# Optimization experiments

Hardware: AMD Instinct MI355X
Metric: run time of the kernel (lower is better)

## Reference

```python
import jax, jax.numpy as jnp
import numpy as np

C = 343.0                      # wave speed
OMEGA = 2.0 * np.pi * 1000.0   # angular frequency
K2 = (C / OMEGA) ** 2          # coefficient on u in the (as-written) residual

N_POINTS = 262144
HIDDEN = 256


def _mlp_point(p, W1, b1, W2, b2, W3, b3, W4, b4):
    # p: (3,) -> scalar u(x,y,z); tanh MLP stand-in for model_estimation
    h = jnp.tanh(p @ W1 + b1)
    h = jnp.tanh(h @ W2 + b2)
    h = jnp.tanh(h @ W3 + b3)
    return (h @ W4 + b4)[0]


def setup_inputs() -> dict:
    key = jax.random.key(0)
    ks = jax.random.split(key, 5)

    def init_w(k, fan_in, fan_out):
        return jax.random.normal(k, (fan_in, fan_out), dtype=jnp.float32) / np.sqrt(fan_in).astype(np.float32)

    inputs = jax.random.normal(ks[0], (N_POINTS, 3), dtype=jnp.float32)
    W1 = init_w(ks[1], 3, HIDDEN)
    W2 = init_w(ks[2], HIDDEN, HIDDEN)
    W3 = init_w(ks[3], HIDDEN, HIDDEN)
    W4 = init_w(ks[4], HIDDEN, 1)
    z = lambda n: jnp.zeros((n,), dtype=jnp.float32)
    return {
        "inputs": inputs,
        "W1": W1, "b1": z(HIDDEN),
        "W2": W2, "b2": z(HIDDEN),
        "W3": W3, "b3": z(HIDDEN),
        "W4": W4, "b4": z(1),
    }


def reference(inputs, W1, b1, W2, b2, W3, b3, W4, b4):
    # Per-point scalar field u(p); Laplacian = trace of the 3x3 Hessian.
    def u_point(p):
        return _mlp_point(p, W1, b1, W2, b2, W3, b3, W4, b4)

    u = jax.vmap(u_point)(inputs)                       # [N]
    hess = jax.vmap(jax.hessian(u_point))(inputs)       # [N, 3, 3]
    laplace_u = hess[:, 0, 0] + hess[:, 1, 1] + hess[:, 2, 2]  # [N]

    pde_residual = laplace_u + K2 * u
    return jnp.mean(jnp.abs(pde_residual) ** 2)
```

## Files before the change

kernel.cpp:

```cpp
#include <hip/hip_runtime.h>
#include <math.h>

#define HID 256
#define PTS 16
#define NSTR 5
#define ROWS (NSTR*PTS)
#define PITCH 272

typedef _Float16 half4v __attribute__((ext_vector_type(4)));
typedef _Float16 half8  __attribute__((ext_vector_type(8)));
typedef float   floatx4 __attribute__((ext_vector_type(4)));

constexpr double PI_D = 3.14159265358979323846;
constexpr float K2F = (float)((343.0/(2.0*PI_D*1000.0))*(343.0/(2.0*PI_D*1000.0)));

__device__ __forceinline__ float tanh_fast(float z) {
  float e = __expf(2.0f*z);
  return 1.0f - 2.0f * __builtin_amdgcn_rcpf(e + 1.0f);
}

__global__ void pack_kernel(const float* __restrict__ W2, const float* __restrict__ W3,
                            _Float16* __restrict__ out) {
  int t = blockIdx.x * blockDim.x + threadIdx.x;
  int l    = t >> 13;
  int rem  = t & 8191;
  int kc   = rem >> 10;
  int nt   = (rem >> 6) & 15;
  int lane = rem & 63;
  const float* W = l ? W3 : W2;
  int k0 = kc*32 + ((lane >> 4) << 3);
  int n  = (nt >> 2)*64 + (lane & 15)*4 + (nt & 3);
  _Float16* o = out + (size_t)t * 8;
  #pragma unroll
  for (int j = 0; j < 8; ++j)
    o[j] = (_Float16)W[(size_t)(k0 + j)*HID + n];
}

__global__ __launch_bounds__(256, 3) void helm_kernel(
    const float* __restrict__ inputs,
    const float* __restrict__ W1, const float* __restrict__ b1,
    const float* __restrict__ b2, const float* __restrict__ b3,
    const float* __restrict__ W4, const float* __restrict__ b4,
    const _Float16* __restrict__ Wpack,
    float* __restrict__ part)
{
  __shared__ __align__(16) _Float16 X[ROWS][PITCH];
  __shared__ float sred[4];

  const int tid  = threadIdx.x;
  const int lane = tid & 63;
  const int wave = tid >> 6;
  const int m    = lane & 15;
  const int q    = lane >> 4;

  const int pbase = blockIdx.x * PTS;

  {
    const int p  = tid >> 4;
    const int c0 = (tid & 15) * 16;
    const float x0 = inputs[(size_t)(pbase + p)*3 + 0];
    const float x1 = inputs[(size_t)(pbase + p)*3 + 1];
    const float x2 = inputs[(size_t)(pbase + p)*3 + 2];
    #pragma unroll
    for (int ch = 0; ch < 2; ++ch) {
      _Float16 o[NSTR][8];
      #pragma unroll
      for (int jj = 0; jj < 2; ++jj) {
        const int n = c0 + ch*8 + jj*4;
        floatx4 w0 = *(const floatx4*)&W1[0*HID + n];
        floatx4 w1 = *(const floatx4*)&W1[1*HID + n];
        floatx4 w2 = *(const floatx4*)&W1[2*HID + n];
        floatx4 bn = *(const floatx4*)&b1[n];
        #pragma unroll
        for (int e = 0; e < 4; ++e) {
          float z  = fmaf(x2, w2[e], fmaf(x1, w1[e], fmaf(x0, w0[e], bn[e])));
          float a  = tanh_fast(z);
          float dd = 1.0f - a*a;
          float wsq = w0[e]*w0[e] + w1[e]*w1[e] + w2[e]*w2[e];
          o[0][jj*4+e] = (_Float16)a;
          o[1][jj*4+e] = (_Float16)(dd*w0[e]);
          o[2][jj*4+e] = (_Float16)(dd*w1[e]);
          o[3][jj*4+e] = (_Float16)(dd*w2[e]);
          o[4][jj*4+e] = (_Float16)(-2.0f*a*dd*wsq);
        }
      }
      #pragma unroll
      for (int s = 0; s < NSTR; ++s)
        *(half8*)(&X[s*PTS + p][c0 + ch*8]) = *(half8*)(o[s]);
    }
  }
  __syncthreads();

  const int colbase = wave*64 + m*4;
  for (int L = 0; L < 2; ++L) {
    const _Float16* Wp = Wpack + (size_t)L * 65536;
    const float* bb = L ? b3 : b2;

    floatx4 acc[NSTR][4];
    #pragma unroll
    for (int s = 0; s < NSTR; ++s)
      #pragma unroll
      for (int c = 0; c < 4; ++c)
        acc[s][c] = (floatx4){0.0f, 0.0f, 0.0f, 0.0f};

    const _Float16* wb = Wp + (((size_t)(wave*4)*64 + lane) << 3);

    half8 bcur[4], bnxt[4];
    #pragma unroll
    for (int c = 0; c < 4; ++c)
      bcur[c] = *(const half8*)(wb + c*512);

    for (int kc = 0; kc < 8; ++kc) {
      const int kn = (kc + 1) & 7;
      #pragma unroll
      for (int c = 0; c < 4; ++c)
        bnxt[c] = *(const half8*)(wb + (size_t)kn*8192 + c*512);
      half8 afrag[NSTR];
      #pragma unroll
      for (int s = 0; s < NSTR; ++s)
        afrag[s] = *(const half8*)(&X[s*PTS + m][kc*32 + q*8]);
      #pragma unroll
      for (int s = 0; s < NSTR; ++s)
        #pragma unroll
        for (int c = 0; c < 4; ++c)
          acc[s][c] = __builtin_amdgcn_mfma_f32_16x16x32_f16(afrag[s], bcur[c], acc[s][c], 0, 0, 0);
      #pragma unroll
      for (int c = 0; c < 4; ++c)
        bcur[c] = bnxt[c];
    }
    __syncthreads();

    floatx4 bv = *(const floatx4*)&bb[colbase];
    #pragma unroll
    for (int r = 0; r < 4; ++r) {
      const int p = q*4 + r;
      _Float16 o[NSTR][4];
      #pragma unroll
      for (int c = 0; c < 4; ++c) {
        float z  = acc[0][c][r] + bv[c];
        float a  = tanh_fast(z);
        float dd = 1.0f - a*a;
        float zp0 = acc[1][c][r], zp1 = acc[2][c][r], zp2 = acc[3][c][r];
        float zpp = acc[4][c][r];
        float s2  = zp0*zp0 + zp1*zp1 + zp2*zp2;
        o[0][c] = (_Float16)a;
        o[1][c] = (_Float16)(dd*zp0);
        o[2][c] = (_Float16)(dd*zp1);
        o[3][c] = (_Float16)(dd*zp2);
        o[4][c] = (_Float16)(fmaf(dd, zpp, -2.0f*a*dd*s2));
      }
      #pragma unroll
      for (int s = 0; s < NSTR; ++s)
        *(half4v*)(&X[s*PTS + p][colbase]) = *(half4v*)(o[s]);
    }
    __syncthreads();
  }

  float resacc = 0.0f;
  #pragma unroll
  for (int pp = 0; pp < 4; ++pp) {
    const int p = wave*4 + pp;
    half4v  xu = *(const half4v*)&X[0*PTS + p][lane*4];
    half4v  xt = *(const half4v*)&X[4*PTS + p][lane*4];
    floatx4 w4 = *(const floatx4*)&W4[lane*4];
    float su = 0.0f, st = 0.0f;
    #pragma unroll
    for (int e = 0; e < 4; ++e) {
      su = fmaf((float)xu[e], w4[e], su);
      st = fmaf((float)xt[e], w4[e], st);
    }
    #pragma unroll
    for (int off = 32; off; off >>= 1) {
      su += __shfl_down(su, off);
      st += __shfl_down(st, off);
    }
    if (lane == 0) {
      float u   = su + b4[0];
      float res = st + K2F * u;
      resacc = fmaf(res, res, resacc);
    }
  }
  if (lane == 0) sred[wave] = resacc;
  __syncthreads();
  if (tid == 0)
    part[blockIdx.x] = sred[0] + sred[1] + sred[2] + sred[3];
}

__global__ void reduce_kernel(const float* __restrict__ part, float* __restrict__ out,
                              int nblk, float scale) {
  float s = 0.0f;
  for (int i = threadIdx.x; i < (nblk >> 2); i += 256) {
    floatx4 v = *(const floatx4*)&part[i << 2];
    s += (v[0] + v[1]) + (v[2] + v[3]);
  }
  #pragma unroll
  for (int off = 32; off; off >>= 1) s += __shfl_down(s, off);
  __shared__ float sm[4];
  if ((threadIdx.x & 63) == 0) sm[threadIdx.x >> 6] = s;
  __syncthreads();
  if (threadIdx.x == 0) out[0] = ((sm[0] + sm[1]) + (sm[2] + sm[3])) * scale;
}

extern "C" void kernel_launch(void* const* d_in, const int* in_sizes, int n_in,
                              void* d_out, int out_size, void* d_ws, size_t ws_size,
                              hipStream_t stream) {
  const float* inputs = (const float*)d_in[0];
  const float* W1 = (const float*)d_in[1];
  const float* b1 = (const float*)d_in[2];
  const float* W2 = (const float*)d_in[3];
  const float* b2 = (const float*)d_in[4];
  const float* W3 = (const float*)d_in[5];
  const float* b3 = (const float*)d_in[6];
  const float* W4 = (const float*)d_in[7];
  const float* b4 = (const float*)d_in[8];
  float* out = (float*)d_out;

  _Float16* wp   = (_Float16*)d_ws;
  float*    part = (float*)((char*)d_ws + 2*65536*2);

  int N    = in_sizes[0] / 3;
  int nblk = N / PTS;

  pack_kernel<<<64, 256, 0, stream>>>(W2, W3, wp);
  helm_kernel<<<nblk, 256, 0, stream>>>(inputs, W1, b1, b2, b3, W4, b4, wp, part);
  reduce_kernel<<<1, 256, 0, stream>>>(part, out, nblk, 1.0f / (float)N);
}
```

Measured before the change: 467.7 us.

## Fuse final layer dot into layer-3 epilogue, unroll k-loop, use packed fp16 converts

The W4 output projection now runs directly on the layer-3 MFMA accumulators in registers, skipping the fp16 write to LDS and the re-read. Partial sums are reduced with shuffles and a small LDS exchange. The k-loop is fully unrolled with direct B-fragment loads in place of the manual double buffer, fp16 stores use packed cvt_pkrtz conversions, and tanh uses exp2 directly. The extra unrolling raises register pressure, which may affect occupancy under the 3-blocks launch bound.

After: 402.4 us. 1.16x faster.

```diff
diff --git a/kernel.cpp b/kernel.cpp
--- a/kernel.cpp
+++ b/kernel.cpp
@@ -7,15 +7,20 @@
 #define ROWS (NSTR*PTS)
 #define PITCH 272
 
-typedef _Float16 half4v __attribute__((ext_vector_type(4)));
+typedef __fp16  fp16x2 __attribute__((ext_vector_type(2)));
 typedef _Float16 half8  __attribute__((ext_vector_type(8)));
 typedef float   floatx4 __attribute__((ext_vector_type(4)));
 
 constexpr double PI_D = 3.14159265358979323846;
 constexpr float K2F = (float)((343.0/(2.0*PI_D*1000.0))*(343.0/(2.0*PI_D*1000.0)));
 
+union H2U { fp16x2 h; unsigned int u; };
+__device__ __forceinline__ unsigned int pk(float a, float b) {
+  H2U t; t.h = __builtin_amdgcn_cvt_pkrtz(a, b); return t.u;
+}
+
 __device__ __forceinline__ float tanh_fast(float z) {
-  float e = __expf(2.0f*z);
+  float e = __builtin_amdgcn_exp2f(z * 2.8853900817779268f);
   return 1.0f - 2.0f * __builtin_amdgcn_rcpf(e + 1.0f);
 }
 
@@ -45,7 +50,6 @@
     float* __restrict__ part)
 {
   __shared__ __align__(16) _Float16 X[ROWS][PITCH];
-  __shared__ float sred[4];
 
   const int tid  = threadIdx.x;
   const int lane = tid & 63;
@@ -63,7 +67,7 @@
     const float x2 = inputs[(size_t)(pbase + p)*3 + 2];
     #pragma unroll
     for (int ch = 0; ch < 2; ++ch) {
-      _Float16 o[NSTR][8];
+      float v[NSTR][8];
       #pragma unroll
       for (int jj = 0; jj < 2; ++jj) {
         const int n = c0 + ch*8 + jj*4;
@@ -76,45 +80,35 @@
           float z  = fmaf(x2, w2[e], fmaf(x1, w1[e], fmaf(x0, w0[e], bn[e])));
           float a  = tanh_fast(z);
           float dd = 1.0f - a*a;
-          float wsq = w0[e]*w0[e] + w1[e]*w1[e] + w2[e]*w2[e];
-          o[0][jj*4+e] = (_Float16)a;
-          o[1][jj*4+e] = (_Float16)(dd*w0[e]);
-          o[2][jj*4+e] = (_Float16)(dd*w1[e]);
-          o[3][jj*4+e] = (_Float16)(dd*w2[e]);
-          o[4][jj*4+e] = (_Float16)(-2.0f*a*dd*wsq);
+          float wsq = fmaf(w0[e], w0[e], fmaf(w1[e], w1[e], w2[e]*w2[e]));
+          v[0][jj*4+e] = a;
+          v[1][jj*4+e] = dd*w0[e];
+          v[2][jj*4+e] = dd*w1[e];
+          v[3][jj*4+e] = dd*w2[e];
+          v[4][jj*4+e] = -2.0f*a*dd*wsq;
         }
       }
       #pragma unroll
-      for (int s = 0; s < NSTR; ++s)
-        *(half8*)(&X[s*PTS + p][c0 + ch*8]) = *(half8*)(o[s]);
+      for (int s = 0; s < NSTR; ++s) {
+        uint4 u;
+        u.x = pk(v[s][0], v[s][1]); u.y = pk(v[s][2], v[s][3]);
+        u.z = pk(v[s][4], v[s][5]); u.w = pk(v[s][6], v[s][7]);
+        *(uint4*)&X[s*PTS + p][c0 + ch*8] = u;
+      }
     }
   }
   __syncthreads();
 
   const int colbase = wave*64 + m*4;
-  for (int L = 0; L < 2; ++L) {
-    const _Float16* Wp = Wpack + (size_t)L * 65536;
-    const float* bb = L ? b3 : b2;
-
-    floatx4 acc[NSTR][4];
-    #pragma unroll
-    for (int s = 0; s < NSTR; ++s)
+
+  auto kloop = [&](const _Float16* __restrict__ Wp, floatx4 (&acc)[NSTR][4]) {
+    const _Float16* wb = Wp + (((size_t)(wave*4)*64 + lane) << 3);
+    #pragma unroll
+    for (int kc = 0; kc < 8; ++kc) {
+      half8 bfrag[4];
       #pragma unroll
       for (int c = 0; c < 4; ++c)
-        acc[s][c] = (floatx4){0.0f, 0.0f, 0.0f, 0.0f};
-
-    const _Float16* wb = Wp + (((size_t)(wave*4)*64 + lane) << 3);
-
-    half8 bcur[4], bnxt[4];
-    #pragma unroll
-    for (int c = 0; c < 4; ++c)
-      bcur[c] = *(const half8*)(wb + c*512);
-
-    for (int kc = 0; kc < 8; ++kc) {
-      const int kn = (kc + 1) & 7;
-      #pragma unroll
-      for (int c = 0; c < 4; ++c)
-        bnxt[c] = *(const half8*)(wb + (size_t)kn*8192 + c*512);
+        bfrag[c] = *(const half8*)(wb + (size_t)kc*8192 + c*512);
       half8 afrag[NSTR];
       #pragma unroll
       for (int s = 0; s < NSTR; ++s)
@@ -123,67 +117,110 @@
       for (int s = 0; s < NSTR; ++s)
         #pragma unroll
         for (int c = 0; c < 4; ++c)
-          acc[s][c] = __builtin_amdgcn_mfma_f32_16x16x32_f16(afrag[s], bcur[c], acc[s][c], 0, 0, 0);
+          acc[s][c] = __builtin_amdgcn_mfma_f32_16x16x32_f16(afrag[s], bfrag[c], acc[s][c], 0, 0, 0);
+    }
+  };
+
+  {
+    floatx4 acc[NSTR][4];
+    #pragma unroll
+    for (int s = 0; s < NSTR; ++s)
       #pragma unroll
       for (int c = 0; c < 4; ++c)
-        bcur[c] = bnxt[c];
-    }
+        acc[s][c] = (floatx4){0.0f, 0.0f, 0.0f, 0.0f};
+    kloop(Wpack, acc);
     __syncthreads();
 
-    floatx4 bv = *(const floatx4*)&bb[colbase];
+    floatx4 bv = *(const floatx4*)&b2[colbase];
     #pragma unroll
     for (int r = 0; r < 4; ++r) {
       const int p = q*4 + r;
-      _Float16 o[NSTR][4];
+      float va[4], vg0[4], vg1[4], vg2[4], vT[4];
       #pragma unroll
       for (int c = 0; c < 4; ++c) {
         float z  = acc[0][c][r] + bv[c];
         float a  = tanh_fast(z);
         float dd = 1.0f - a*a;
-        float zp0 = acc[1][c][r], zp1 = acc[2][c][r], zp2 = acc[3][c][r];
+        float z0 = acc[1][c][r], z1 = acc[2][c][r], z2 = acc[3][c][r];
         float zpp = acc[4][c][r];
-        float s2  = zp0*zp0 + zp1*zp1 + zp2*zp2;
-        o[0][c] = (_Float16)a;
-        o[1][c] = (_Float16)(dd*zp0);
-        o[2][c] = (_Float16)(dd*zp1);
-        o[3][c] = (_Float16)(dd*zp2);
-        o[4][c] = (_Float16)(fmaf(dd, zpp, -2.0f*a*dd*s2));
-      }
-      #pragma unroll
-      for (int s = 0; s < NSTR; ++s)
-        *(half4v*)(&X[s*PTS + p][colbase]) = *(half4v*)(o[s]);
+        float s2 = fmaf(z0, z0, fmaf(z1, z1, z2*z2));
+        va[c]  = a;
+        vg0[c] = dd*z0; vg1[c] = dd*z1; vg2[c] = dd*z2;
+        vT[c]  = fmaf(dd, zpp, -2.0f*a*dd*s2);
+      }
+      uint2 u;
+      u.x = pk(va[0],va[1]);   u.y = pk(va[2],va[3]);   *(uint2*)&X[0*PTS + p][colbase] = u;
+      u.x = pk(vg0[0],vg0[1]); u.y = pk(vg0[2],vg0[3]); *(uint2*)&X[1*PTS + p][colbase] = u;
+      u.x = pk(vg1[0],vg1[1]); u.y = pk(vg1[2],vg1[3]); *(uint2*)&X[2*PTS + p][colbase] = u;
+      u.x = pk(vg2[0],vg2[1]); u.y = pk(vg2[2],vg2[3]); *(uint2*)&X[3*PTS + p][colbase] = u;
+      u.x = pk(vT[0],vT[1]);   u.y = pk(vT[2],vT[3]);   *(uint2*)&X[4*PTS + p][colbase] = u;
     }
     __syncthreads();
   }
 
-  float resacc = 0.0f;
-  #pragma unroll
-  for (int pp = 0; pp < 4; ++pp) {
-    const int p = wave*4 + pp;
-    half4v  xu = *(const half4v*)&X[0*PTS + p][lane*4];
-    half4v  xt = *(const half4v*)&X[4*PTS + p][lane*4];
-    floatx4 w4 = *(const floatx4*)&W4[lane*4];
-    float su = 0.0f, st = 0.0f;
-    #pragma unroll
-    for (int e = 0; e < 4; ++e) {
-      su = fmaf((float)xu[e], w4[e], su);
-      st = fmaf((float)xt[e], w4[e], st);
-    }
-    #pragma unroll
-    for (int off = 32; off; off >>= 1) {
-      su += __shfl_down(su, off);
-      st += __shfl_down(st, off);
-    }
-    if (lane == 0) {
-      float u   = su + b4[0];
-      float res = st + K2F * u;
-      resacc = fmaf(res, res, resacc);
-    }
-  }
-  if (lane == 0) sred[wave] = resacc;
+  {
+    floatx4 acc[NSTR][4];
+    #pragma unroll
+    for (int s = 0; s < NSTR; ++s)
+      #pragma unroll
+      for (int c = 0; c < 4; ++c)
+        acc[s][c] = (floatx4){0.0f, 0.0f, 0.0f, 0.0f};
+    kloop(Wpack + 65536, acc);
+    __syncthreads();
+
+    floatx4 bv = *(const floatx4*)&b3[colbase];
+    floatx4 w4 = *(const floatx4*)&W4[colbase];
+    float su[4] = {0,0,0,0}, st[4] = {0,0,0,0};
+    #pragma unroll
+    for (int r = 0; r < 4; ++r)
+      #pragma unroll
+      for (int c = 0; c < 4; ++c) {
+        float z  = acc[0][c][r] + bv[c];
+        float a  = tanh_fast(z);
+        float dd = 1.0f - a*a;
+        float z0 = acc[1][c][r], z1 = acc[2][c][r], z2 = acc[3][c][r];
+        float zpp = acc[4][c][r];
+        float s2 = fmaf(z0, z0, fmaf(z1, z1, z2*z2));
+        float T  = fmaf(dd, zpp, -2.0f*a*dd*s2);
+        su[r] = fmaf(a, w4[c], su[r]);
+        st[r] = fmaf(T, w4[c], st[r]);
+      }
+
+    #pragma unroll
+    for (int off = 8; off >= 1; off >>= 1)
+      #pragma unroll
+      for (int r = 0; r < 4; ++r) {
+        su[r] += __shfl_down(su[r], off);
+        st[r] += __shfl_down(st[r], off);
+      }
+    float* S = (float*)X;
+    if (m == 0) {
+      #pragma unroll
+      for (int r = 0; r < 4; ++r) {
+        S[(q*4 + r)*8 + wave]     = su[r];
+        S[(q*4 + r)*8 + 4 + wave] = st[r];
+      }
+    }
+  }
   __syncthreads();
-  if (tid == 0)
-    part[blockIdx.x] = sred[0] + sred[1] + sred[2] + sred[3];
+
+  if (wave == 0) {
+    const float* S = (const float*)X;
+    int pidx = lane >> 2, w = lane & 3;
+    float suc = S[pidx*8 + w];
+    float stc = S[pidx*8 + 4 + w];
+    suc += __shfl_down(suc, 1); suc += __shfl_down(suc, 2);
+    stc += __shfl_down(stc, 1); stc += __shfl_down(stc, 2);
+    float sq = 0.0f;
+    if ((lane & 3) == 0) {
+      float u   = suc + b4[0];
+      float res = fmaf(K2F, u, stc);
+      sq = res * res;
+    }
+    sq += __shfl_down(sq, 4); sq += __shfl_down(sq, 8);
+    sq += __shfl_down(sq, 16); sq += __shfl_down(sq, 32);
+    if (lane == 0) part[blockIdx.x] = sq;
+  }
 }
 
 __global__ void reduce_kernel(const float* __restrict__ part, float* __restrict__ out,
```
